# Performance work log

Measured on AMD Instinct MI355X. Metric: run time of the kernel, lower is better.

Reference implementation:

```python
import jax, jax.numpy as jnp
import numpy as np

FS = 24000.0
C_SOUND = 343.0
MAX_TAU = 6
IGNORE = -100
PAIRS = np.array([(0, 1), (0, 2), (0, 3), (1, 2), (1, 3), (2, 3)])  # m1<m2 loop order
PERMS_NP = np.array([(0, 1, 2), (0, 2, 1), (1, 0, 2), (1, 2, 0), (2, 0, 1), (2, 1, 0)])  # itertools order


def _mic_locs():
    # [rad, azi_deg, ele_deg] per mic, centered at origin (matches center_mic_coords)
    coords = np.array([[0.042, 45, 35], [0.042, -45, -35], [0.042, 135, -35], [0.042, -135, 35]], dtype=np.float64)
    rad = coords[:, 0]
    azi = coords[:, 1] * 2 * np.pi / 360
    ele = coords[:, 2] * 2 * np.pi / 360
    locs = np.stack([rad * np.cos(azi) * np.cos(ele), rad * np.sin(azi) * np.cos(ele), rad * np.sin(ele)], axis=1)
    return jnp.asarray(locs, dtype=jnp.float32)

MIC_LOCS = _mic_locs()  # [4,3]


def _get_tdoa_targets(target):
    """Vectorized get_tdoa_target. target: [B,T,E,5,C].
    Assumes <=1 active class per (b,t,track) so the random class shuffle is a no-op.
    Returns (tdoas, tdoas2) as int32 [B,T,E,6]."""
    B, T, E, F, C = target.shape
    active = target[:, :, :, 0, :]                                  # [B,T,E,C] 0/1 flags
    is_active = jnp.any(active > 0, axis=-1)                        # [B,T,E]
    doa = jnp.einsum('btec,btedc->bted', active, target[:, :, :, 1:4, :])  # [B,T,E,3]
    dist = jnp.einsum('btec,btec->bte', active, target[:, :, :, 4, :])     # [B,T,E]
    src = doa * dist[..., None]                                     # [B,T,E,3]
    d = jnp.linalg.norm(src[..., None, :] - MIC_LOCS, axis=-1)      # [B,T,E,4] dist to each mic
    tdoa = d[..., PAIRS[:, 0]] - d[..., PAIRS[:, 1]]                # [B,T,E,6]
    tdoa = jnp.round(tdoa * FS / C_SOUND) + MAX_TAU                 # [B,T,E,6]
    # compact active tracks to the front (stable keeps track order, matching tr_cnt)
    order = jnp.argsort(jnp.logical_not(is_active), axis=-1)        # [B,T,E]
    gathered = jnp.take_along_axis(tdoa, order[..., None], axis=2)  # [B,T,E,6]
    n = jnp.sum(is_active, axis=-1)                                 # [B,T] number of events
    k = jnp.arange(E)[None, None, :]                                # slot index
    idx1 = jnp.clip(jnp.minimum(k, n[:, :, None] - 1), 0, E - 1)    # pad with LAST event
    idx2 = jnp.where(k < n[:, :, None], k, 0)                       # pad with FIRST event
    tdoas = jnp.take_along_axis(gathered, idx1[..., None], axis=2)
    tdoas2 = jnp.take_along_axis(gathered, idx2[..., None], axis=2)
    empty = (n == 0)[:, :, None, None]
    tdoas = jnp.where(empty, float(IGNORE), tdoas)
    tdoas2 = jnp.where(empty, float(IGNORE), tdoas2)
    return tdoas.astype(jnp.int32), tdoas2.astype(jnp.int32)


def _forward(pred, t_a, t_b):
    B, T, C, Tr, ntd = pred.shape
    N = B * T * ntd
    p = pred.transpose(0, 1, 4, 2, 3).reshape(N, C, Tr)             # [N,C,Tr]
    ta = t_a.transpose(0, 1, 3, 2).reshape(N, Tr)                   # [N,Tr]
    tb = t_b.transpose(0, 1, 3, 2).reshape(N, Tr)
    logp = jax.nn.log_softmax(p, axis=1)                            # [N,C,Tr]
    perms = jnp.asarray(PERMS_NP)                                   # [6,Tr]
    ar = jnp.arange(Tr)

    def pit(t):
        tc = jnp.clip(t, 0, C - 1)
        # L[n,i,j] = CE(pred track j, target track i); ignore_index -> 0
        L = -jnp.take_along_axis(logp, jnp.broadcast_to(tc[:, :, None], (N, Tr, Tr)), axis=1)
        L = jnp.where((t == IGNORE)[:, :, None], 0.0, L)
        pl = L[:, ar[None, :], perms].mean(axis=-1)                 # [N,6] per-perm mean loss
        pidx = jnp.argmin(pl, axis=1)                               # first min (matches torch loop)
        return jnp.take_along_axis(pl, pidx[:, None], axis=1)[:, 0], perms[pidx]

    loss1, perm1 = pit(ta)
    loss2, perm2 = pit(tb)
    use2 = loss2 < loss1                                            # torch.min keeps first on ties
    loss = jnp.where(use2, loss2, loss1)
    t_sel = jnp.where(use2[:, None], tb, ta)
    perm_sel = jnp.where(use2[:, None], perm2, perm1)

    pred_cls = jnp.argmax(p, axis=1)                                # [N,Tr]
    t_perm = jnp.take_along_axis(t_sel, perm_sel, axis=1)           # target reordered by opt perm
    valid = t_perm != IGNORE
    npred = jnp.sum(valid)
    correct = jnp.sum((pred_cls == t_perm) & valid)
    acc = jnp.where(npred > 0, correct.astype(jnp.float32) / jnp.maximum(npred, 1).astype(jnp.float32), 0.0)

    mask = loss > 0.0
    nval = jnp.sum(mask)
    lmean = jnp.where(nval > 0, jnp.sum(jnp.where(mask, loss, 0.0)) / jnp.maximum(nval, 1).astype(loss.dtype), 0.0)
    return lmean, acc


def setup_inputs() -> dict:
    key = jax.random.key(0)
    B, T, E, NCLS, NTD, CPRED = 128, 600, 3, 13, 6, 13
    k1, k2, k3, k4, k5 = jax.random.split(key, 5)
    pred = jax.random.normal(k1, (B, T, CPRED, E, NTD), dtype=jnp.float32)
    act_cls = jax.random.randint(k2, (B, T, E), 0, NCLS)
    act_flag = (jax.random.uniform(k3, (B, T, E)) < 0.5).astype(jnp.float32)
    onehot = jax.nn.one_hot(act_cls, NCLS, dtype=jnp.float32) * act_flag[..., None]  # <=1 active class/track
    doa = jax.random.normal(k4, (B, T, E, 3), dtype=jnp.float32)
    doa = doa / jnp.linalg.norm(doa, axis=-1, keepdims=True)
    dist = jax.random.uniform(k5, (B, T, E), minval=1.0, maxval=3.0, dtype=jnp.float32)
    target = jnp.concatenate([
        onehot[:, :, :, None, :],
        jnp.broadcast_to(doa[..., None], (B, T, E, 3, NCLS)),
        jnp.broadcast_to(dist[..., None, None], (B, T, E, 1, NCLS)),
    ], axis=3).astype(jnp.float32)                                  # [B,T,E,5,NCLS]
    return {"pred": pred, "target": target}


def reference(pred, target):
    t_a, t_b = _get_tdoa_targets(target)
    return _forward(pred, t_a, t_b)
```

## Files before the change

### kernel.cpp

```cpp
#include <hip/hip_runtime.h>
#include <cstdint>
#include <cstddef>

#define BT_TOTAL 76800
#define NCLS 13
#define IGN  (-100)

#define CPB   16
#define NBLK  (BT_TOTAL / CPB)
#define NTHR  128
#define ITEMS (CPB * 6)
#define NF4T  (CPB * 195 / 4)
#define KT    7
#define NF4P  (CPB * 234 / 4)
#define KP    8

struct Partial { float ls; int lc; int cor; int val; };

__device__ __forceinline__ void stage16(const float4* __restrict__ g, float4* l) {
    __builtin_amdgcn_global_load_lds((const __attribute__((address_space(1))) void*)g,
                                     (__attribute__((address_space(3))) void*)l,
                                     16, 0, 0);
}

extern "C" __global__ __launch_bounds__(NTHR)
void tdoa_fused(const float* __restrict__ pred, const float* __restrict__ target,
                Partial* __restrict__ part) {
    const int tid = threadIdx.x;
    const int cb  = blockIdx.x * CPB;

    __shared__ float4 sT4[NF4T];
    __shared__ float4 sP4[NF4P];
    __shared__ uint32_t sTd[CPB * 12];
    const float* sT = (const float*)sT4;
    const float* sP = (const float*)sP4;

    {
        const float4* gt = (const float4*)(target + (size_t)cb * 195);
#pragma unroll
        for (int k = 0; k < KT; k++) {
            const int i = k * NTHR + tid;
            if (i < NF4T) stage16(gt + i, &sT4[i]);
        }
        const float4* gp = (const float4*)(pred + (size_t)cb * 234);
#pragma unroll
        for (int k = 0; k < KP; k++) {
            const int i = k * NTHR + tid;
            if (i < NF4P) stage16(gp + i, &sP4[i]);
        }
    }
    __syncthreads();

    if (tid < CPB) {
        const float* tg = sT + tid * 195;

        const float MX[4] = { 0.02432757455f,  0.02432757455f, -0.02432757455f, -0.02432757455f };
        const float MY[4] = { 0.02432757455f, -0.02432757455f,  0.02432757455f, -0.02432757455f };
        const float MZ[4] = { 0.02409021033f, -0.02409021033f, -0.02409021033f,  0.02409021033f };
        const int PI_[6] = {0,0,0,1,1,2};
        const int PJ_[6] = {1,2,3,2,3,3};

        int  td[3][6];
        bool ab[3];
        int  nact = 0;
#pragma unroll
        for (int e = 0; e < 3; e++) {
            float a[NCLS];
#pragma unroll
            for (int c = 0; c < NCLS; c++) a[c] = tg[e * 65 + c];
            bool ia = false;
#pragma unroll
            for (int c = 0; c < NCLS; c++) ia = ia || (a[c] > 0.0f);
            float d0 = 0.f, d1 = 0.f, d2 = 0.f, ds = 0.f;
#pragma unroll
            for (int c = 0; c < NCLS; c++) {
                d0 += a[c] * tg[e * 65 + 13 + c];
                d1 += a[c] * tg[e * 65 + 26 + c];
                d2 += a[c] * tg[e * 65 + 39 + c];
                ds += a[c] * tg[e * 65 + 52 + c];
            }
            const float sx = d0 * ds, sy = d1 * ds, sz = d2 * ds;
            float dm[4];
#pragma unroll
            for (int m = 0; m < 4; m++) {
                const float ex = sx - MX[m], ey = sy - MY[m], ez = sz - MZ[m];
                dm[m] = sqrtf(ex * ex + ey * ey + ez * ez);
            }
#pragma unroll
            for (int p = 0; p < 6; p++) {
                const float diff = dm[PI_[p]] - dm[PJ_[p]];
                td[e][p] = (int)rintf((diff * 24000.0f) / 343.0f) + 6;
            }
            ab[e] = ia;
            nact += ia ? 1 : 0;
        }

        const int o0 = ab[0] ? 0 : (ab[1] ? 1 : 2);
        const int o1 = (ab[0] && ab[1]) ? 1 : 2;
        const bool empty = (nact == 0);

#pragma unroll
        for (int p = 0; p < 6; p++) {
            const int g0 = (o0 == 0) ? td[0][p] : ((o0 == 1) ? td[1][p] : td[2][p]);
            const int g1 = (o1 == 1) ? td[1][p] : td[2][p];
            const int g2 = td[2][p];
            int ta0 = g0;
            int ta1 = (nact >= 2) ? g1 : g0;
            int ta2 = (nact == 3) ? g2 : ((nact == 2) ? g1 : g0);
            int tb0 = g0;
            int tb1 = (nact >= 2) ? g1 : g0;
            int tb2 = (nact == 3) ? g2 : g0;
            uint32_t w0 = (uint32_t)(ta0 & 0xff) | ((uint32_t)(ta1 & 0xff) << 8) | ((uint32_t)(ta2 & 0xff) << 16);
            uint32_t w1 = (uint32_t)(tb0 & 0xff) | ((uint32_t)(tb1 & 0xff) << 8) | ((uint32_t)(tb2 & 0xff) << 16);
            if (empty) { w0 = 0x009c9c9cu; w1 = 0x009c9c9cu; }
            sTd[tid * 12 + p * 2 + 0] = w0;
            sTd[tid * 12 + p * 2 + 1] = w1;
        }
    }
    __syncthreads();

    float lsum = 0.f;
    int   lcnt = 0, cor = 0, nval = 0;

    if (tid < ITEMS) {
        const int btl = tid / 6;
        const int p   = tid - btl * 6;
        const float* pp = sP + btl * 234 + p;

        float x[NCLS][3];
#pragma unroll
        for (int c = 0; c < NCLS; c++)
#pragma unroll
            for (int j = 0; j < 3; j++)
                x[c][j] = pp[c * 18 + j * 6];

        int   am[3];
        float lse[3];
#pragma unroll
        for (int j = 0; j < 3; j++) {
            float m = x[0][j]; int a = 0;
#pragma unroll
            for (int c = 1; c < NCLS; c++) { if (x[c][j] > m) { m = x[c][j]; a = c; } }
            float s = 0.f;
#pragma unroll
            for (int c = 0; c < NCLS; c++) s += expf(x[c][j] - m);
            am[j] = a; lse[j] = m + logf(s);
        }

        const uint32_t w0 = sTd[btl * 12 + p * 2 + 0];
        const uint32_t w1 = sTd[btl * 12 + p * 2 + 1];
        int ta[3], tb[3];
#pragma unroll
        for (int i = 0; i < 3; i++) {
            ta[i] = (int)(int8_t)(w0 >> (8 * i));
            tb[i] = (int)(int8_t)(w1 >> (8 * i));
        }

        float La[3][3], Lb[3][3];
#pragma unroll
        for (int i = 0; i < 3; i++) {
            const int  ca  = (ta[i] < 0) ? 0 : ta[i];
            const int  cb2 = (tb[i] < 0) ? 0 : tb[i];
            const bool ia  = (ta[i] == IGN);
            const bool ib  = (tb[i] == IGN);
#pragma unroll
            for (int j = 0; j < 3; j++) {
                La[i][j] = ia ? 0.f : (lse[j] - pp[ca  * 18 + j * 6]);
                Lb[i][j] = ib ? 0.f : (lse[j] - pp[cb2 * 18 + j * 6]);
            }
        }

        const int P0[6] = {0,0,1,1,2,2};
        const int P1[6] = {1,2,0,2,0,1};
        const int P2[6] = {2,1,2,0,1,0};
        float l1 = 0.f, l2 = 0.f; int i1 = 0, i2 = 0;
#pragma unroll
        for (int q = 0; q < 6; q++) {
            const float va = (La[0][P0[q]] + La[1][P1[q]] + La[2][P2[q]]) * (1.0f / 3.0f);
            const float vb = (Lb[0][P0[q]] + Lb[1][P1[q]] + Lb[2][P2[q]]) * (1.0f / 3.0f);
            if (q == 0) { l1 = va; l2 = vb; }
            else {
                if (va < l1) { l1 = va; i1 = q; }
                if (vb < l2) { l2 = vb; i2 = q; }
            }
        }

        const bool use2 = (l2 < l1);
        const float loss = use2 ? l2 : l1;
        const int  qsel = use2 ? i2 : i1;
        const int PK[6] = {36, 24, 33, 9, 18, 6};
        int pk = PK[0];
#pragma unroll
        for (int k = 1; k < 6; k++) pk = (qsel == k) ? PK[k] : pk;
        const int s0 = use2 ? tb[0] : ta[0];
        const int s1 = use2 ? tb[1] : ta[1];
        const int s2 = use2 ? tb[2] : ta[2];
#pragma unroll
        for (int i = 0; i < 3; i++) {
            const int pi = (pk >> (2 * i)) & 3;
            const int tp = (pi == 0) ? s0 : ((pi == 1) ? s1 : s2);
            const bool v = (tp != IGN);
            nval += v ? 1 : 0;
            cor  += (v && (am[i] == tp)) ? 1 : 0;
        }
        if (loss > 0.f) { lsum += loss; lcnt++; }
    }

#pragma unroll
    for (int off = 32; off > 0; off >>= 1) {
        lsum += __shfl_down(lsum, off, 64);
        lcnt += __shfl_down(lcnt, off, 64);
        cor  += __shfl_down(cor,  off, 64);
        nval += __shfl_down(nval, off, 64);
    }
    __shared__ float rf[2];
    __shared__ int   r1[2], r2[2], r3[2];
    const int wid = tid >> 6;
    if ((tid & 63) == 0) { rf[wid] = lsum; r1[wid] = lcnt; r2[wid] = cor; r3[wid] = nval; }
    __syncthreads();
    if (tid == 0) {
        Partial pt;
        pt.ls  = rf[0] + rf[1];
        pt.lc  = r1[0] + r1[1];
        pt.cor = r2[0] + r2[1];
        pt.val = r3[0] + r3[1];
        part[blockIdx.x] = pt;
    }
}

extern "C" __global__ __launch_bounds__(256)
void tdoa_final(const Partial* __restrict__ part, float* __restrict__ out) {
    const int tid = threadIdx.x;
    double ls = 0.0; int lc = 0, cor = 0, val = 0;
    for (int i = tid; i < NBLK; i += 256) {
        const Partial p = part[i];
        ls += (double)p.ls; lc += p.lc; cor += p.cor; val += p.val;
    }
#pragma unroll
    for (int off = 32; off > 0; off >>= 1) {
        ls  += __shfl_down(ls,  off, 64);
        lc  += __shfl_down(lc,  off, 64);
        cor += __shfl_down(cor, off, 64);
        val += __shfl_down(val, off, 64);
    }
    __shared__ double sd[4];
    __shared__ int    s1[4], s2[4], s3[4];
    const int wid = tid >> 6;
    if ((tid & 63) == 0) { sd[wid] = ls; s1[wid] = lc; s2[wid] = cor; s3[wid] = val; }
    __syncthreads();
    if (tid == 0) {
        const double L = sd[0] + sd[1] + sd[2] + sd[3];
        const int c1 = s1[0] + s1[1] + s1[2] + s1[3];
        const int c2 = s2[0] + s2[1] + s2[2] + s2[3];
        const int c3 = s3[0] + s3[1] + s3[2] + s3[3];
        out[0] = (c1 > 0) ? (float)(L / (double)c1) : 0.0f;
        out[1] = (c3 > 0) ? ((float)c2 / (float)c3) : 0.0f;
    }
}

extern "C" void kernel_launch(void* const* d_in, const int* in_sizes, int n_in,
                              void* d_out, int out_size, void* d_ws, size_t ws_size,
                              hipStream_t stream) {
    const float* pred   = (const float*)d_in[0];
    const float* target = (const float*)d_in[1];
    Partial* part = (Partial*)d_ws;
    float* out = (float*)d_out;
    hipLaunchKernelGGL(tdoa_fused, dim3(NBLK), dim3(NTHR), 0, stream, pred, target, part);
    hipLaunchKernelGGL(tdoa_final, dim3(1),    dim3(256), 0, stream, part, out);
}
```

Measured before the change: 164.1 us.

## Double-buffer LDS staging in single-wave persistent blocks looping over chunks

Each block becomes a single 64-lane wave that walks 8 chunks of 8 cells. It prefetches the next chunk into a second LDS buffer with global_load_lds and waits with an explicit vmcnt before computing the current chunk. Target-TDOA computation is spread across 24 lanes (one per cell-track) and broadcast with shuffles instead of running serially in 16 threads. The cross-wave shared-memory reduction and the block barriers are gone. The risks are the hand-written vmcnt count, the change in clamping behaviour, and the lower number of blocks reducing parallelism.

```diff
diff --git a/kernel.cpp b/kernel.cpp
--- a/kernel.cpp
+++ b/kernel.cpp
@@ -6,204 +6,216 @@
 #define NCLS 13
 #define IGN  (-100)
 
-#define CPB   16
-#define NBLK  (BT_TOTAL / CPB)
-#define NTHR  128
-#define ITEMS (CPB * 6)
+#define CPB   8
+#define NCH   8
+#define NTHR  64
+#define CELLS_PER_BLK (CPB * NCH)
+#define NBLK  (BT_TOTAL / CELLS_PER_BLK)
+
 #define NF4T  (CPB * 195 / 4)
 #define KT    7
+#define PADT  (KT * 64)
 #define NF4P  (CPB * 234 / 4)
 #define KP    8
+#define PADP  (KP * 64)
 
 struct Partial { float ls; int lc; int cor; int val; };
 
-__device__ __forceinline__ void stage16(const float4* __restrict__ g, float4* l) {
+__device__ __forceinline__ void stage16(const float4* g, float4* l) {
     __builtin_amdgcn_global_load_lds((const __attribute__((address_space(1))) void*)g,
                                      (__attribute__((address_space(3))) void*)l,
                                      16, 0, 0);
 }
 
+__device__ __forceinline__ void issue_chunk(const float* __restrict__ target,
+                                            const float* __restrict__ pred,
+                                            int cell0, float4* bT, float4* bP, int lane) {
+    const float4* gt = (const float4*)(target + (size_t)cell0 * 195);
+#pragma unroll
+    for (int r = 0; r < KT; r++) {
+        const int i  = r * 64 + lane;
+        const int ic = (i < NF4T) ? i : (NF4T - 1);
+        stage16(gt + ic, bT + i);
+    }
+    const float4* gp = (const float4*)(pred + (size_t)cell0 * 234);
+#pragma unroll
+    for (int r = 0; r < KP; r++) {
+        const int i  = r * 64 + lane;
+        const int ic = (i < NF4P) ? i : (NF4P - 1);
+        stage16(gp + ic, bP + i);
+    }
+}
+
 extern "C" __global__ __launch_bounds__(NTHR)
 void tdoa_fused(const float* __restrict__ pred, const float* __restrict__ target,
                 Partial* __restrict__ part) {
-    const int tid = threadIdx.x;
-    const int cb  = blockIdx.x * CPB;
-
-    __shared__ float4 sT4[NF4T];
-    __shared__ float4 sP4[NF4P];
-    __shared__ uint32_t sTd[CPB * 12];
-    const float* sT = (const float*)sT4;
-    const float* sP = (const float*)sP4;
-
-    {
-        const float4* gt = (const float4*)(target + (size_t)cb * 195);
-#pragma unroll
-        for (int k = 0; k < KT; k++) {
-            const int i = k * NTHR + tid;
-            if (i < NF4T) stage16(gt + i, &sT4[i]);
-        }
-        const float4* gp = (const float4*)(pred + (size_t)cb * 234);
-#pragma unroll
-        for (int k = 0; k < KP; k++) {
-            const int i = k * NTHR + tid;
-            if (i < NF4P) stage16(gp + i, &sP4[i]);
-        }
-    }
-    __syncthreads();
-
-    if (tid < CPB) {
-        const float* tg = sT + tid * 195;
-
-        const float MX[4] = { 0.02432757455f,  0.02432757455f, -0.02432757455f, -0.02432757455f };
-        const float MY[4] = { 0.02432757455f, -0.02432757455f,  0.02432757455f, -0.02432757455f };
-        const float MZ[4] = { 0.02409021033f, -0.02409021033f, -0.02409021033f,  0.02409021033f };
-        const int PI_[6] = {0,0,0,1,1,2};
-        const int PJ_[6] = {1,2,3,2,3,3};
-
-        int  td[3][6];
-        bool ab[3];
-        int  nact = 0;
-#pragma unroll
-        for (int e = 0; e < 3; e++) {
-            float a[NCLS];
-#pragma unroll
-            for (int c = 0; c < NCLS; c++) a[c] = tg[e * 65 + c];
-            bool ia = false;
-#pragma unroll
-            for (int c = 0; c < NCLS; c++) ia = ia || (a[c] > 0.0f);
-            float d0 = 0.f, d1 = 0.f, d2 = 0.f, ds = 0.f;
-#pragma unroll
-            for (int c = 0; c < NCLS; c++) {
-                d0 += a[c] * tg[e * 65 + 13 + c];
-                d1 += a[c] * tg[e * 65 + 26 + c];
-                d2 += a[c] * tg[e * 65 + 39 + c];
-                ds += a[c] * tg[e * 65 + 52 + c];
-            }
-            const float sx = d0 * ds, sy = d1 * ds, sz = d2 * ds;
-            float dm[4];
-#pragma unroll
-            for (int m = 0; m < 4; m++) {
-                const float ex = sx - MX[m], ey = sy - MY[m], ez = sz - MZ[m];
-                dm[m] = sqrtf(ex * ex + ey * ey + ez * ez);
-            }
-#pragma unroll
-            for (int p = 0; p < 6; p++) {
-                const float diff = dm[PI_[p]] - dm[PJ_[p]];
-                td[e][p] = (int)rintf((diff * 24000.0f) / 343.0f) + 6;
-            }
-            ab[e] = ia;
-            nact += ia ? 1 : 0;
-        }
-
-        const int o0 = ab[0] ? 0 : (ab[1] ? 1 : 2);
-        const int o1 = (ab[0] && ab[1]) ? 1 : 2;
-        const bool empty = (nact == 0);
-
-#pragma unroll
-        for (int p = 0; p < 6; p++) {
-            const int g0 = (o0 == 0) ? td[0][p] : ((o0 == 1) ? td[1][p] : td[2][p]);
-            const int g1 = (o1 == 1) ? td[1][p] : td[2][p];
-            const int g2 = td[2][p];
-            int ta0 = g0;
-            int ta1 = (nact >= 2) ? g1 : g0;
-            int ta2 = (nact == 3) ? g2 : ((nact == 2) ? g1 : g0);
-            int tb0 = g0;
-            int tb1 = (nact >= 2) ? g1 : g0;
-            int tb2 = (nact == 3) ? g2 : g0;
-            uint32_t w0 = (uint32_t)(ta0 & 0xff) | ((uint32_t)(ta1 & 0xff) << 8) | ((uint32_t)(ta2 & 0xff) << 16);
-            uint32_t w1 = (uint32_t)(tb0 & 0xff) | ((uint32_t)(tb1 & 0xff) << 8) | ((uint32_t)(tb2 & 0xff) << 16);
-            if (empty) { w0 = 0x009c9c9cu; w1 = 0x009c9c9cu; }
-            sTd[tid * 12 + p * 2 + 0] = w0;
-            sTd[tid * 12 + p * 2 + 1] = w1;
-        }
-    }
-    __syncthreads();
+    const int lane     = threadIdx.x;
+    const int cellbase = blockIdx.x * CELLS_PER_BLK;
+
+    __shared__ float4 sT0[PADT], sT1[PADT];
+    __shared__ float4 sP0[PADP], sP1[PADP];
 
     float lsum = 0.f;
     int   lcnt = 0, cor = 0, nval = 0;
 
-    if (tid < ITEMS) {
-        const int btl = tid / 6;
-        const int p   = tid - btl * 6;
-        const float* pp = sP + btl * 234 + p;
-
-        float x[NCLS][3];
-#pragma unroll
-        for (int c = 0; c < NCLS; c++)
-#pragma unroll
-            for (int j = 0; j < 3; j++)
-                x[c][j] = pp[c * 18 + j * 6];
-
-        int   am[3];
-        float lse[3];
-#pragma unroll
-        for (int j = 0; j < 3; j++) {
-            float m = x[0][j]; int a = 0;
-#pragma unroll
-            for (int c = 1; c < NCLS; c++) { if (x[c][j] > m) { m = x[c][j]; a = c; } }
-            float s = 0.f;
-#pragma unroll
-            for (int c = 0; c < NCLS; c++) s += expf(x[c][j] - m);
-            am[j] = a; lse[j] = m + logf(s);
+    issue_chunk(target, pred, cellbase, sT0, sP0, lane);
+
+#pragma unroll
+    for (int k = 0; k < NCH; k++) {
+        float4*      nT = (k & 1) ? sT0 : sT1;
+        float4*      nP = (k & 1) ? sP0 : sP1;
+        const float* cT = (const float*)((k & 1) ? sT1 : sT0);
+        const float* cP = (const float*)((k & 1) ? sP1 : sP0);
+
+        if (k + 1 < NCH) {
+            issue_chunk(target, pred, cellbase + (k + 1) * CPB, nT, nP, lane);
+            asm volatile("s_waitcnt vmcnt(15)" ::: "memory");
+        } else {
+            asm volatile("s_waitcnt vmcnt(0)" ::: "memory");
         }
-
-        const uint32_t w0 = sTd[btl * 12 + p * 2 + 0];
-        const uint32_t w1 = sTd[btl * 12 + p * 2 + 1];
-        int ta[3], tb[3];
-#pragma unroll
-        for (int i = 0; i < 3; i++) {
-            ta[i] = (int)(int8_t)(w0 >> (8 * i));
-            tb[i] = (int)(int8_t)(w1 >> (8 * i));
+        __builtin_amdgcn_sched_barrier(0);
+
+        uint32_t tdw = 0;
+        {
+            const int cellA = lane / 3;
+            const int e     = lane - cellA * 3;
+            if (lane < 24) {
+                const float* tg = cT + cellA * 195 + e * 65;
+                float a[NCLS];
+#pragma unroll
+                for (int c = 0; c < NCLS; c++) a[c] = tg[c];
+                bool ia = false;
+#pragma unroll
+                for (int c = 0; c < NCLS; c++) ia = ia || (a[c] > 0.0f);
+                float d0 = 0.f, d1 = 0.f, d2 = 0.f, ds = 0.f;
+#pragma unroll
+                for (int c = 0; c < NCLS; c++) {
+                    d0 += a[c] * tg[13 + c];
+                    d1 += a[c] * tg[26 + c];
+                    d2 += a[c] * tg[39 + c];
+                    ds += a[c] * tg[52 + c];
+                }
+                const float sx = d0 * ds, sy = d1 * ds, sz = d2 * ds;
+                const float MX[4] = { 0.02432757455f,  0.02432757455f, -0.02432757455f, -0.02432757455f };
+                const float MY[4] = { 0.02432757455f, -0.02432757455f,  0.02432757455f, -0.02432757455f };
+                const float MZ[4] = { 0.02409021033f, -0.02409021033f, -0.02409021033f,  0.02409021033f };
+                float dm[4];
+#pragma unroll
+                for (int m = 0; m < 4; m++) {
+                    const float ex = sx - MX[m], ey = sy - MY[m], ez = sz - MZ[m];
+                    dm[m] = sqrtf(ex * ex + ey * ey + ez * ez);
+                }
+                const int PI_[6] = {0,0,0,1,1,2};
+                const int PJ_[6] = {1,2,3,2,3,3};
+                uint32_t w = 0;
+#pragma unroll
+                for (int p = 0; p < 6; p++) {
+                    int t = (int)rintf((dm[PI_[p]] - dm[PJ_[p]]) * (24000.0f / 343.0f)) + 6;
+                    t = (t < 0) ? 0 : ((t > 12) ? 12 : t);
+                    w |= ((uint32_t)t) << (4 * p);
+                }
+                if (ia) w |= (1u << 28);
+                tdw = w;
+            }
         }
 
-        float La[3][3], Lb[3][3];
-#pragma unroll
-        for (int i = 0; i < 3; i++) {
-            const int  ca  = (ta[i] < 0) ? 0 : ta[i];
-            const int  cb2 = (tb[i] < 0) ? 0 : tb[i];
-            const bool ia  = (ta[i] == IGN);
-            const bool ib  = (tb[i] == IGN);
+        const int btl48 = (lane < 48) ? (lane / 6) : 0;
+        const uint32_t t0 = __shfl(tdw, btl48 * 3 + 0, 64);
+        const uint32_t t1 = __shfl(tdw, btl48 * 3 + 1, 64);
+        const uint32_t t2 = __shfl(tdw, btl48 * 3 + 2, 64);
+
+        if (lane < 48) {
+            const int btl = lane / 6;
+            const int p   = lane - btl * 6;
+
+            const bool ab0 = (t0 >> 28) & 1, ab1 = (t1 >> 28) & 1, ab2 = (t2 >> 28) & 1;
+            const int  nact = (int)ab0 + (int)ab1 + (int)ab2;
+            const int  v0 = (int)((t0 >> (4 * p)) & 15);
+            const int  v1 = (int)((t1 >> (4 * p)) & 15);
+            const int  v2 = (int)((t2 >> (4 * p)) & 15);
+            const int  g0 = ab0 ? v0 : (ab1 ? v1 : v2);
+            const int  g1 = (ab0 && ab1) ? v1 : v2;
+            const int  g2 = v2;
+            int ta[3], tb[3];
+            ta[0] = g0;
+            ta[1] = (nact >= 2) ? g1 : g0;
+            ta[2] = (nact == 3) ? g2 : ((nact == 2) ? g1 : g0);
+            tb[0] = g0;
+            tb[1] = (nact >= 2) ? g1 : g0;
+            tb[2] = (nact == 3) ? g2 : g0;
+            if (nact == 0) { ta[0]=ta[1]=ta[2]=IGN; tb[0]=tb[1]=tb[2]=IGN; }
+
+            const float* pp = cP + btl * 234 + p;
+
+            float x[NCLS][3];
+#pragma unroll
+            for (int c = 0; c < NCLS; c++)
+#pragma unroll
+                for (int j = 0; j < 3; j++)
+                    x[c][j] = pp[c * 18 + j * 6];
+
+            int   am[3];
+            float lse[3];
 #pragma unroll
             for (int j = 0; j < 3; j++) {
-                La[i][j] = ia ? 0.f : (lse[j] - pp[ca  * 18 + j * 6]);
-                Lb[i][j] = ib ? 0.f : (lse[j] - pp[cb2 * 18 + j * 6]);
-            }
+                float m = x[0][j]; int a = 0;
+#pragma unroll
+                for (int c = 1; c < NCLS; c++) { if (x[c][j] > m) { m = x[c][j]; a = c; } }
+                float s = 0.f;
+#pragma unroll
+                for (int c = 0; c < NCLS; c++) s += expf(x[c][j] - m);
+                am[j] = a; lse[j] = m + logf(s);
+            }
+
+            float La[3][3], Lb[3][3];
+#pragma unroll
+            for (int i = 0; i < 3; i++) {
+                const int  ca  = (ta[i] < 0) ? 0 : ta[i];
+                const int  cbb = (tb[i] < 0) ? 0 : tb[i];
+                const bool ia2 = (ta[i] == IGN);
+                const bool ib2 = (tb[i] == IGN);
+#pragma unroll
+                for (int j = 0; j < 3; j++) {
+                    La[i][j] = ia2 ? 0.f : (lse[j] - pp[ca  * 18 + j * 6]);
+                    Lb[i][j] = ib2 ? 0.f : (lse[j] - pp[cbb * 18 + j * 6]);
+                }
+            }
+
+            const int P0[6] = {0,0,1,1,2,2};
+            const int P1[6] = {1,2,0,2,0,1};
+            const int P2[6] = {2,1,2,0,1,0};
+            float l1 = 0.f, l2 = 0.f; int i1 = 0, i2 = 0;
+#pragma unroll
+            for (int q = 0; q < 6; q++) {
+                const float va = (La[0][P0[q]] + La[1][P1[q]] + La[2][P2[q]]) * (1.0f / 3.0f);
+                const float vb = (Lb[0][P0[q]] + Lb[1][P1[q]] + Lb[2][P2[q]]) * (1.0f / 3.0f);
+                if (q == 0) { l1 = va; l2 = vb; }
+                else {
+                    if (va < l1) { l1 = va; i1 = q; }
+                    if (vb < l2) { l2 = vb; i2 = q; }
+                }
+            }
+
+            const bool use2 = (l2 < l1);
+            const float loss = use2 ? l2 : l1;
+            const int  qsel = use2 ? i2 : i1;
+            const int PK[6] = {36, 24, 33, 9, 18, 6};
+            int pk = PK[0];
+#pragma unroll
+            for (int kk = 1; kk < 6; kk++) pk = (qsel == kk) ? PK[kk] : pk;
+            const int s0 = use2 ? tb[0] : ta[0];
+            const int s1 = use2 ? tb[1] : ta[1];
+            const int s2 = use2 ? tb[2] : ta[2];
+#pragma unroll
+            for (int i = 0; i < 3; i++) {
+                const int pi = (pk >> (2 * i)) & 3;
+                const int tp = (pi == 0) ? s0 : ((pi == 1) ? s1 : s2);
+                const bool v = (tp != IGN);
+                nval += v ? 1 : 0;
+                cor  += (v && (am[i] == tp)) ? 1 : 0;
+            }
+            if (loss > 0.f) { lsum += loss; lcnt++; }
         }
-
-        const int P0[6] = {0,0,1,1,2,2};
-        const int P1[6] = {1,2,0,2,0,1};
-        const int P2[6] = {2,1,2,0,1,0};
-        float l1 = 0.f, l2 = 0.f; int i1 = 0, i2 = 0;
-#pragma unroll
-        for (int q = 0; q < 6; q++) {
-            const float va = (La[0][P0[q]] + La[1][P1[q]] + La[2][P2[q]]) * (1.0f / 3.0f);
-            const float vb = (Lb[0][P0[q]] + Lb[1][P1[q]] + Lb[2][P2[q]]) * (1.0f / 3.0f);
-            if (q == 0) { l1 = va; l2 = vb; }
-            else {
-                if (va < l1) { l1 = va; i1 = q; }
-                if (vb < l2) { l2 = vb; i2 = q; }
-            }
-        }
-
-        const bool use2 = (l2 < l1);
-        const float loss = use2 ? l2 : l1;
-        const int  qsel = use2 ? i2 : i1;
-        const int PK[6] = {36, 24, 33, 9, 18, 6};
-        int pk = PK[0];
-#pragma unroll
-        for (int k = 1; k < 6; k++) pk = (qsel == k) ? PK[k] : pk;
-        const int s0 = use2 ? tb[0] : ta[0];
-        const int s1 = use2 ? tb[1] : ta[1];
-        const int s2 = use2 ? tb[2] : ta[2];
-#pragma unroll
-        for (int i = 0; i < 3; i++) {
-            const int pi = (pk >> (2 * i)) & 3;
-            const int tp = (pi == 0) ? s0 : ((pi == 1) ? s1 : s2);
-            const bool v = (tp != IGN);
-            nval += v ? 1 : 0;
-            cor  += (v && (am[i] == tp)) ? 1 : 0;
-        }
-        if (loss > 0.f) { lsum += loss; lcnt++; }
     }
 
 #pragma unroll
@@ -213,17 +225,8 @@
         cor  += __shfl_down(cor,  off, 64);
         nval += __shfl_down(nval, off, 64);
     }
-    __shared__ float rf[2];
-    __shared__ int   r1[2], r2[2], r3[2];
-    const int wid = tid >> 6;
-    if ((tid & 63) == 0) { rf[wid] = lsum; r1[wid] = lcnt; r2[wid] = cor; r3[wid] = nval; }
-    __syncthreads();
-    if (tid == 0) {
-        Partial pt;
-        pt.ls  = rf[0] + rf[1];
-        pt.lc  = r1[0] + r1[1];
-        pt.cor = r2[0] + r2[1];
-        pt.val = r3[0] + r3[1];
+    if (lane == 0) {
+        Partial pt; pt.ls = lsum; pt.lc = lcnt; pt.cor = cor; pt.val = nval;
         part[blockIdx.x] = pt;
     }
 }
```

New measurement: 176.7 us. +7.6%, slower.
